# Kernel tuning notes

Hardware: AMD Instinct MI355X
Metric: run time of the kernel (lower is better)

Reference implementation:

```python
import jax, jax.numpy as jnp
import numpy as np

B, E, N, NREL, K, T, L = 8, 2000, 10000, 25, 16, 3, 32
TAU1 = 10.0

def _clip01(x):
    return jnp.clip(x, 0.0, 1.0)

def setup_inputs():
    key = jax.random.key(0)
    ks = jax.random.split(key, 10)
    ent = jax.random.randint(ks[0], (B,), 0, E)
    input_x = jnp.zeros((B, E), jnp.float32).at[jnp.arange(B), ent].set(1.0)
    tidx = jax.random.randint(ks[1], (E,), 0, K)
    type_mat = jnp.zeros((E, K), jnp.float32).at[jnp.arange(E), tidx].set(1.0)
    heads = jax.random.randint(ks[2], (N,), 0, E)
    tails = jax.random.randint(ks[3], (N,), 0, E)
    rels = jax.random.randint(ks[4], (N,), 0, NREL)
    e2triple = jnp.zeros((E, N), jnp.float32).at[heads, jnp.arange(N)].set(1.0)
    triple2e = jnp.zeros((N, E), jnp.float32).at[jnp.arange(N), tails].set(1.0)
    triple2r = jnp.zeros((N, NREL), jnp.float32).at[jnp.arange(N), rels].set(1.0)
    def ku(k, shape):
        fan_in = int(np.prod(shape[1:]))
        bnd = 1.0 / np.sqrt(fan_in)
        return jax.random.uniform(k, shape, jnp.float32, -bnd, bnd)
    w = ku(ks[5], (T, L, NREL))
    weight = ku(ks[6], (L, 1))
    h = jnp.ones((T, L, NREL - 1), jnp.float32)
    h_x = jnp.ones((L, NREL - 1), jnp.float32)
    h_type = ku(ks[7], (T, L, K))
    h_x_type = ku(ks[8], (L, K))
    alpha = jnp.ones((T, L), jnp.float32)
    beta = jnp.ones((T, L), jnp.float32)
    alpha_x = jnp.ones((L,), jnp.float32)
    beta_x = jnp.ones((L,), jnp.float32)
    return dict(input_x=input_x, type_mat=type_mat, e2triple=e2triple,
                triple2e=triple2e, triple2r=triple2r, w=w, weight=weight,
                h=h, h_x=h_x, h_type=h_type, h_x_type=h_x_type,
                alpha=alpha, beta=beta, alpha_x=alpha_x, beta_x=beta_x, flag=0)

def _forward(input_x, type_mat, e2triple, triple2e, triple2r, w, weight,
             h, h_x, h_type, h_x_type, alpha, beta, alpha_x, beta_x):
    # flag=False, is_training=False path of TCLMModel.forward
    Bb = input_x.shape[0]
    Nn, Ee = triple2e.shape
    Tt, Ll = alpha.shape
    nrel = w.shape[-1]
    half = (nrel - 1) // 2
    x_ori = input_x @ e2triple                      # [B,N]
    e2r = triple2e.T @ triple2r                     # [E,nrel]
    hidden_base = _clip01(e2r)[:, :-1]              # [E,nrel-1]
    hx_raw = _clip01(x_ori @ triple2r)              # [B,nrel]
    hidden_x_base = jnp.concatenate([hx_raw[:, half:-1], hx_raw[:, :half]], axis=-1)
    ax = _clip01(alpha_x / TAU1)
    bx = _clip01(beta_x / TAU1)
    gate_x = 1.0 - _clip01(ax + bx)                 # [L]
    hxp = _clip01(h_x / TAU1)                       # [L,nrel-1]
    hxtp = _clip01(h_x_type / TAU1)                 # [L,K]
    hidden_type_x = input_x @ (type_mat @ hxtp.T)   # [B,L]
    hx_lin = hidden_x_base @ hxp.T                  # [B,L]
    s = None
    for t in range(Tt):
        a = _clip01(alpha[t] / TAU1)                # [L]
        b = _clip01(beta[t] / TAU1)
        hp = _clip01(h[t] / TAU1)                   # [L,nrel-1]
        htp = _clip01(h_type[t] / TAU1)             # [L,K]
        hidden = _clip01(a[None] * (type_mat @ htp.T) + b[None] * (hidden_base @ hp.T))
        hidden = (hidden + (1.0 - _clip01(a + b))[None]).T        # [L,E]
        # note: original code uses alpha/beta (not alpha_x/beta_x) here; replicate
        hidden_x = _clip01(a[None] * hidden_type_x + b[None] * hx_lin) + gate_x[None]  # [B,L]
        w_probs = jax.nn.softmax(w[t], axis=-1)     # [L,nrel]
        srel = triple2r @ w_probs.T                 # [N,L]
        if t == 0:
            sc = x_ori[:, None, :] * srel.T[None]   # [B,L,N]
            s = (sc.reshape(-1, Nn) @ triple2e).reshape(Bb, Ll, Ee)
            s = s * hidden[None] * hidden_x[:, :, None]
        else:
            xprev = (s.reshape(-1, Ee) @ e2triple).reshape(Bb, Ll, Nn)
            sc = xprev * srel.T[None]               # [B,L,N]
            s = (sc.reshape(-1, Nn) @ triple2e).reshape(Bb, Ll, Ee)
            s = s * hidden[None]
    out = jnp.einsum('ble,lk->bek', s, jnp.tanh(weight))[..., 0]  # [B,E]
    return out

def reference(input_x, type_mat, e2triple, triple2e, triple2r, w, weight,
              h, h_x, h_type, h_x_type, alpha, beta, alpha_x, beta_x, flag):
    return _forward(input_x, type_mat, e2triple, triple2e, triple2r, w, weight,
                    h, h_x, h_type, h_x_type, alpha, beta, alpha_x, beta_x)
```

## Files before the change

### kernel.cpp

```cpp
#include <hip/hip_runtime.h>

#define B 8
#define E 2000
#define NTRI 10000
#define NRELS 25
#define KT 16
#define TT 3
#define LL 32
#define TAU1 10.0f
#define XBLK 8192
#define XTHR 256
#define LCAP 256

typedef __attribute__((ext_vector_type(4))) float f32x4;

__device__ __forceinline__ float clip01(float x) { return fminf(fmaxf(x, 0.0f), 1.0f); }

__global__ void __launch_bounds__(XTHR) extract_all(
        const f32x4* __restrict__ e2t, const f32x4* __restrict__ t2e,
        const float4* __restrict__ t2r, const float4* __restrict__ ix,
        const float4* __restrict__ tm, const float* __restrict__ w,
        int* __restrict__ heads, int* __restrict__ tails, int* __restrict__ rels,
        int* __restrict__ ent, int* __restrict__ tidx,
        unsigned int* __restrict__ mask_g, int* __restrict__ cnt_g,
        float* __restrict__ wrow_g, float4* __restrict__ out4) {
    const int gtid = blockIdx.x * XTHR + threadIdx.x;
    const int gs = XBLK * XTHR;

    if (gtid < 2048) mask_g[gtid] = 0u;
    if (gtid < 64) cnt_g[gtid] = 0;
    float4 z = make_float4(0.f, 0.f, 0.f, 0.f);
    for (int i = gtid; i < B * E / 4; i += gs) out4[i] = z;

    if (gtid < TT * LL) {
        const float* wr = w + gtid * NRELS;
        float mx = wr[0];
        for (int r = 1; r < NRELS; r++) mx = fmaxf(mx, wr[r]);
        float ex[NRELS], s = 0.f;
        for (int r = 0; r < NRELS; r++) { ex[r] = expf(wr[r] - mx); s += ex[r]; }
        float inv = 1.f / s;
        for (int r = 0; r < NRELS; r++) wrow_g[gtid * NRELS + r] = ex[r] * inv;
    }

    for (int i = gtid; i < B * E / 4; i += gs) {
        float4 v = ix[i];
        if (v.x != 0.f || v.y != 0.f || v.z != 0.f || v.w != 0.f) {
            float c[4] = {v.x, v.y, v.z, v.w};
#pragma unroll
            for (int k = 0; k < 4; k++)
                if (c[k] != 0.f) { int a = i * 4 + k; int bq = a / E; ent[bq] = a - bq * E; }
        }
    }
    for (int i = gtid; i < E * KT / 4; i += gs) {
        float4 v = tm[i];
        if (v.x != 0.f || v.y != 0.f || v.z != 0.f || v.w != 0.f) {
            float c[4] = {v.x, v.y, v.z, v.w};
#pragma unroll
            for (int k = 0; k < 4; k++)
                if (c[k] != 0.f) { int a = i * 4 + k; int e = a / KT; tidx[e] = a - e * KT; }
        }
    }
    for (int i = gtid; i < NTRI * NRELS / 4; i += gs) {
        float4 v = t2r[i];
        if (v.x != 0.f || v.y != 0.f || v.z != 0.f || v.w != 0.f) {
            float c[4] = {v.x, v.y, v.z, v.w};
#pragma unroll
            for (int k = 0; k < 4; k++)
                if (c[k] != 0.f) { int a = i * 4 + k; int j = a / NRELS; rels[j] = a - j * NRELS; }
        }
    }
    for (int i = gtid; i < E * NTRI / 4; i += gs) {
        f32x4 va = __builtin_nontemporal_load(&e2t[i]);
        f32x4 vb = __builtin_nontemporal_load(&t2e[i]);
        if (va.x != 0.f || va.y != 0.f || va.z != 0.f || va.w != 0.f) {
            float c[4] = {va.x, va.y, va.z, va.w};
#pragma unroll
            for (int k = 0; k < 4; k++)
                if (c[k] != 0.f) { int a = i * 4 + k; int hd = a / NTRI; heads[a - hd * NTRI] = hd; }
        }
        if (vb.x != 0.f || vb.y != 0.f || vb.z != 0.f || vb.w != 0.f) {
            float c[4] = {vb.x, vb.y, vb.z, vb.w};
#pragma unroll
            for (int k = 0; k < 4; k++)
                if (c[k] != 0.f) { int a = i * 4 + k; int j = a / E; tails[j] = a - j * E; }
        }
    }
}

__global__ void __launch_bounds__(256) build_aux(
        const int* __restrict__ heads, const int* __restrict__ tails,
        const int* __restrict__ rels, const int* __restrict__ ent,
        unsigned int* __restrict__ mask_g, int* __restrict__ cnt_g,
        int* __restrict__ list_g) {
    int j = blockIdx.x * 256 + threadIdx.x;
    if (j >= NTRI) return;
    int r = rels[j];
    if (r < NRELS - 1) atomicOr(&mask_g[tails[j]], 1u << r);
    int hd = heads[j];
#pragma unroll
    for (int q = 0; q < B; q++) {
        if (hd == ent[q]) {
            int p = atomicAdd(&cnt_g[q], 1);
            if (p < LCAP) list_g[q * LCAP + p] = j;
        }
    }
}

__global__ void __launch_bounds__(512) mega_prop(
        const int* __restrict__ heads, const int* __restrict__ tails,
        const int* __restrict__ rels, const int* __restrict__ ent,
        const int* __restrict__ tidx,
        const unsigned int* __restrict__ mask_g, const int* __restrict__ cnt_g,
        const int* __restrict__ list_g, const float* __restrict__ wrow_g,
        const float* __restrict__ h, const float* __restrict__ h_type,
        const float* __restrict__ alpha, const float* __restrict__ beta,
        const float* __restrict__ h_x, const float* __restrict__ h_x_type,
        const float* __restrict__ alpha_x, const float* __restrict__ beta_x,
        const float* __restrict__ weight, float* __restrict__ out) {
    __shared__ float prev_s[E];
    __shared__ float acc_s[E];
    __shared__ unsigned int mask_s[E];
    __shared__ int tidx_s[E];
    __shared__ float wrow_s[NRELS];
    __shared__ float hp_s[NRELS - 1];
    __shared__ float htp_s[KT];
    __shared__ float extra_sh;

    const int NT = 512;
    const int bI = blockIdx.x >> 5, l = blockIdx.x & 31, tid = threadIdx.x;
    const int ent_b = ent[bI];
    const int cnt = min(cnt_g[bI], LCAP);

    for (int e = tid; e < E; e += NT) {
        acc_s[e] = 0.f;
        mask_s[e] = mask_g[e];
        tidx_s[e] = tidx[e];
    }

    const uint4* h4 = (const uint4*)heads;
    const uint4* t4 = (const uint4*)tails;
    const uint4* r4 = (const uint4*)rels;

    for (int t = 0; t < TT; t++) {
        const int tl = t * LL + l;
        if (tid < NRELS) wrow_s[tid] = wrow_g[tl * NRELS + tid];
        if (tid >= 64 && tid < 64 + NRELS - 1)
            hp_s[tid - 64] = clip01(h[tl * (NRELS - 1) + (tid - 64)] / TAU1);
        if (tid >= 128 && tid < 128 + KT)
            htp_s[tid - 128] = clip01(h_type[tl * KT + (tid - 128)] / TAU1);
        __syncthreads();

        if (t == 0) {
            for (int i = tid; i < cnt; i += NT) {
                int j = list_g[bI * LCAP + i];
                atomicAdd(&acc_s[tails[j]], wrow_s[rels[j]]);
            }
        } else {
            for (int i = tid; i < NTRI / 4; i += NT) {
                uint4 hh = h4[i];
                float p0 = prev_s[hh.x], p1 = prev_s[hh.y];
                float p2 = prev_s[hh.z], p3 = prev_s[hh.w];
                if (p0 != 0.f || p1 != 0.f || p2 != 0.f || p3 != 0.f) {
                    uint4 tv = t4[i], rr = r4[i];
                    if (p0 != 0.f) atomicAdd(&acc_s[tv.x], p0 * wrow_s[rr.x]);
                    if (p1 != 0.f) atomicAdd(&acc_s[tv.y], p1 * wrow_s[rr.y]);
                    if (p2 != 0.f) atomicAdd(&acc_s[tv.z], p2 * wrow_s[rr.z]);
                    if (p3 != 0.f) atomicAdd(&acc_s[tv.w], p3 * wrow_s[rr.w]);
                }
            }
        }
        __syncthreads();

        const float a = clip01(alpha[tl] / TAU1);
        const float bb = clip01(beta[tl] / TAU1);
        const float base = 1.f - clip01(a + bb);

        if (t == 0 && tid == 0) {
            unsigned int fl = 0u;
            for (int i = 0; i < cnt; i++) fl |= 1u << rels[list_g[bI * LCAP + i]];
            float hxlin = 0.f;
            for (int i = 0; i < NRELS - 1; i++) {
                int pi = (i < 12) ? (12 + i) : (i - 12);
                if ((fl >> pi) & 1u) hxlin += clip01(h_x[l * (NRELS - 1) + i] / TAU1);
            }
            float htx = clip01(h_x_type[l * KT + tidx_s[ent_b]] / TAU1);
            float ax = clip01(alpha_x[l] / TAU1), bx = clip01(beta_x[l] / TAU1);
            extra_sh = clip01(a * htx + bb * hxlin) + (1.f - clip01(ax + bx));
        }
        __syncthreads();

        const float extra = (t == 0) ? extra_sh : 1.f;

        if (t < TT - 1) {
            for (int e = tid; e < E; e += NT) {
                unsigned int m = mask_s[e];
                float dot = 0.f;
#pragma unroll
                for (int i = 0; i < NRELS - 1; i++) dot += ((m >> i) & 1u) ? hp_s[i] : 0.f;
                float he = clip01(a * htp_s[tidx_s[e]] + bb * dot) + base;
                prev_s[e] = acc_s[e] * he * extra;
                acc_s[e] = 0.f;
            }
        } else {
            float tw = tanhf(weight[l]);
            for (int e = tid; e < E; e += NT) {
                unsigned int m = mask_s[e];
                float dot = 0.f;
#pragma unroll
                for (int i = 0; i < NRELS - 1; i++) dot += ((m >> i) & 1u) ? hp_s[i] : 0.f;
                float he = clip01(a * htp_s[tidx_s[e]] + bb * dot) + base;
                atomicAdd(&out[bI * E + e], acc_s[e] * he * tw);
            }
        }
        __syncthreads();
    }
}

extern "C" void kernel_launch(void* const* d_in, const int* in_sizes, int n_in,
                              void* d_out, int out_size, void* d_ws, size_t ws_size,
                              hipStream_t stream) {
    const float4* ix       = (const float4*)d_in[0];
    const float4* tm       = (const float4*)d_in[1];
    const f32x4*  e2t      = (const f32x4*)d_in[2];
    const f32x4*  t2e      = (const f32x4*)d_in[3];
    const float4* t2r      = (const float4*)d_in[4];
    const float*  w        = (const float*)d_in[5];
    const float*  weight   = (const float*)d_in[6];
    const float*  h        = (const float*)d_in[7];
    const float*  h_x      = (const float*)d_in[8];
    const float*  h_type   = (const float*)d_in[9];
    const float*  h_x_type = (const float*)d_in[10];
    const float*  alpha    = (const float*)d_in[11];
    const float*  beta     = (const float*)d_in[12];
    const float*  alpha_x  = (const float*)d_in[13];
    const float*  beta_x   = (const float*)d_in[14];
    (void)in_sizes; (void)n_in; (void)out_size; (void)ws_size;

    char* ws = (char*)d_ws;
    int* heads = (int*)ws;
    int* tails = heads + 10048;
    int* rels  = tails + 10048;
    int* ent   = rels + 10048;
    int* tidx  = ent + 64;
    unsigned int* mask_g = (unsigned int*)(tidx + 2048);
    int* cnt_g = (int*)(mask_g + 2048);
    int* list_g = cnt_g + 64;
    float* wrow_g = (float*)(list_g + B * LCAP);

    extract_all<<<XBLK, XTHR, 0, stream>>>(e2t, t2e, t2r, ix, tm, w,
                                           heads, tails, rels, ent, tidx,
                                           mask_g, cnt_g, wrow_g, (float4*)d_out);

    build_aux<<<(NTRI + 255) / 256, 256, 0, stream>>>(heads, tails, rels, ent,
                                                      mask_g, cnt_g, list_g);

    mega_prop<<<B * LL, 512, 0, stream>>>(heads, tails, rels, ent, tidx,
                                          mask_g, cnt_g, list_g, wrow_g,
                                          h, h_type, alpha, beta, h_x, h_x_type,
                                          alpha_x, beta_x, weight, (float*)d_out);
}
```

Measured before the change: 212.3 us.

## Precompute per-batch reachable-triple frontier lists for sparse propagation

Adds a per-batch build kernel that performs BFS-style reachability over the triple graph for three hops. It writes packed (head, tail, rel) lists of only the triples that can carry nonzero mass, plus the relation flags for the start entity. The propagation kernel then walks these compact lists instead of scanning all triples at hops 2 and 3, and skips zero-valued atomic adds to the output. The trade-off is a serial build kernel with only 8 blocks and a larger workspace. The packing assumes tail ids fit in 11 bits and that head ids shifted left by 16 stay within int range.

```diff
diff --git a/kernel.cpp b/kernel.cpp
--- a/kernel.cpp
+++ b/kernel.cpp
@@ -10,7 +10,6 @@
 #define TAU1 10.0f
 #define XBLK 8192
 #define XTHR 256
-#define LCAP 256
 
 typedef __attribute__((ext_vector_type(4))) float f32x4;
 
@@ -22,13 +21,10 @@
         const float4* __restrict__ tm, const float* __restrict__ w,
         int* __restrict__ heads, int* __restrict__ tails, int* __restrict__ rels,
         int* __restrict__ ent, int* __restrict__ tidx,
-        unsigned int* __restrict__ mask_g, int* __restrict__ cnt_g,
         float* __restrict__ wrow_g, float4* __restrict__ out4) {
     const int gtid = blockIdx.x * XTHR + threadIdx.x;
     const int gs = XBLK * XTHR;
 
-    if (gtid < 2048) mask_g[gtid] = 0u;
-    if (gtid < 64) cnt_g[gtid] = 0;
     float4 z = make_float4(0.f, 0.f, 0.f, 0.f);
     for (int i = gtid; i < B * E / 4; i += gs) out4[i] = z;
 
@@ -87,31 +83,75 @@
     }
 }
 
-__global__ void __launch_bounds__(256) build_aux(
+__global__ void __launch_bounds__(1024) build_all(
         const int* __restrict__ heads, const int* __restrict__ tails,
         const int* __restrict__ rels, const int* __restrict__ ent,
         unsigned int* __restrict__ mask_g, int* __restrict__ cnt_g,
-        int* __restrict__ list_g) {
-    int j = blockIdx.x * 256 + threadIdx.x;
-    if (j >= NTRI) return;
-    int r = rels[j];
-    if (r < NRELS - 1) atomicOr(&mask_g[tails[j]], 1u << r);
-    int hd = heads[j];
-#pragma unroll
-    for (int q = 0; q < B; q++) {
-        if (hd == ent[q]) {
-            int p = atomicAdd(&cnt_g[q], 1);
-            if (p < LCAP) list_g[q * LCAP + p] = j;
-        }
-    }
+        unsigned int* __restrict__ relflag_g, int* __restrict__ list_g) {
+    __shared__ unsigned int mask_s[E];
+    __shared__ unsigned int reachA[64], reachB[64];
+    __shared__ int cnt_s[TT];
+    __shared__ unsigned int rf;
+    const int b = blockIdx.x, tid = threadIdx.x;
+    const int eb = ent[b];
+
+    if (tid < 64) { reachA[tid] = 0u; reachB[tid] = 0u; }
+    if (tid < TT) cnt_s[tid] = 0;
+    if (tid == 0) rf = 0u;
+
+    if (b == 0) {
+        for (int e = tid; e < E; e += 1024) mask_s[e] = 0u;
+        __syncthreads();
+        for (int j = tid; j < NTRI; j += 1024) {
+            int r = rels[j];
+            if (r < NRELS - 1) atomicOr(&mask_s[tails[j]], 1u << r);
+        }
+        __syncthreads();
+        for (int e = tid; e < E; e += 1024) mask_g[e] = mask_s[e];
+    }
+    __syncthreads();
+
+    int* l1 = list_g + (0 * B + b) * NTRI;
+    int* l2 = list_g + (1 * B + b) * NTRI;
+    int* l3 = list_g + (2 * B + b) * NTRI;
+
+    for (int j = tid; j < NTRI; j += 1024) {
+        if (heads[j] == eb) {
+            int ta = tails[j], r = rels[j];
+            int p = atomicAdd(&cnt_s[0], 1);
+            l1[p] = (eb << 16) | (ta << 5) | r;
+            atomicOr(&reachA[ta >> 5], 1u << (ta & 31));
+            atomicOr(&rf, 1u << r);
+        }
+    }
+    __syncthreads();
+    for (int j = tid; j < NTRI; j += 1024) {
+        int hd = heads[j];
+        if ((reachA[hd >> 5] >> (hd & 31)) & 1u) {
+            int ta = tails[j];
+            int p = atomicAdd(&cnt_s[1], 1);
+            l2[p] = (hd << 16) | (ta << 5) | rels[j];
+            atomicOr(&reachB[ta >> 5], 1u << (ta & 31));
+        }
+    }
+    __syncthreads();
+    for (int j = tid; j < NTRI; j += 1024) {
+        int hd = heads[j];
+        if ((reachB[hd >> 5] >> (hd & 31)) & 1u) {
+            int p = atomicAdd(&cnt_s[2], 1);
+            l3[p] = (hd << 16) | (tails[j] << 5) | rels[j];
+        }
+    }
+    __syncthreads();
+    if (tid < TT) cnt_g[b * 4 + tid] = cnt_s[tid];
+    if (tid == 0) relflag_g[b] = rf;
 }
 
 __global__ void __launch_bounds__(512) mega_prop(
-        const int* __restrict__ heads, const int* __restrict__ tails,
-        const int* __restrict__ rels, const int* __restrict__ ent,
-        const int* __restrict__ tidx,
+        const int* __restrict__ ent, const int* __restrict__ tidx,
         const unsigned int* __restrict__ mask_g, const int* __restrict__ cnt_g,
-        const int* __restrict__ list_g, const float* __restrict__ wrow_g,
+        const unsigned int* __restrict__ relflag_g, const int* __restrict__ list_g,
+        const float* __restrict__ wrow_g,
         const float* __restrict__ h, const float* __restrict__ h_type,
         const float* __restrict__ alpha, const float* __restrict__ beta,
         const float* __restrict__ h_x, const float* __restrict__ h_x_type,
@@ -129,17 +169,12 @@
     const int NT = 512;
     const int bI = blockIdx.x >> 5, l = blockIdx.x & 31, tid = threadIdx.x;
     const int ent_b = ent[bI];
-    const int cnt = min(cnt_g[bI], LCAP);
 
     for (int e = tid; e < E; e += NT) {
         acc_s[e] = 0.f;
         mask_s[e] = mask_g[e];
         tidx_s[e] = tidx[e];
     }
-
-    const uint4* h4 = (const uint4*)heads;
-    const uint4* t4 = (const uint4*)tails;
-    const uint4* r4 = (const uint4*)rels;
 
     for (int t = 0; t < TT; t++) {
         const int tl = t * LL + l;
@@ -150,23 +185,19 @@
             htp_s[tid - 128] = clip01(h_type[tl * KT + (tid - 128)] / TAU1);
         __syncthreads();
 
+        const int cnt = cnt_g[bI * 4 + t];
+        const int* lst = list_g + (t * B + bI) * NTRI;
         if (t == 0) {
             for (int i = tid; i < cnt; i += NT) {
-                int j = list_g[bI * LCAP + i];
-                atomicAdd(&acc_s[tails[j]], wrow_s[rels[j]]);
+                int pk = lst[i];
+                atomicAdd(&acc_s[(pk >> 5) & 2047], wrow_s[pk & 31]);
             }
         } else {
-            for (int i = tid; i < NTRI / 4; i += NT) {
-                uint4 hh = h4[i];
-                float p0 = prev_s[hh.x], p1 = prev_s[hh.y];
-                float p2 = prev_s[hh.z], p3 = prev_s[hh.w];
-                if (p0 != 0.f || p1 != 0.f || p2 != 0.f || p3 != 0.f) {
-                    uint4 tv = t4[i], rr = r4[i];
-                    if (p0 != 0.f) atomicAdd(&acc_s[tv.x], p0 * wrow_s[rr.x]);
-                    if (p1 != 0.f) atomicAdd(&acc_s[tv.y], p1 * wrow_s[rr.y]);
-                    if (p2 != 0.f) atomicAdd(&acc_s[tv.z], p2 * wrow_s[rr.z]);
-                    if (p3 != 0.f) atomicAdd(&acc_s[tv.w], p3 * wrow_s[rr.w]);
-                }
+            for (int i = tid; i < cnt; i += NT) {
+                int pk = lst[i];
+                float pv = prev_s[pk >> 16];
+                if (pv != 0.f)
+                    atomicAdd(&acc_s[(pk >> 5) & 2047], pv * wrow_s[pk & 31]);
             }
         }
         __syncthreads();
@@ -176,8 +207,7 @@
         const float base = 1.f - clip01(a + bb);
 
         if (t == 0 && tid == 0) {
-            unsigned int fl = 0u;
-            for (int i = 0; i < cnt; i++) fl |= 1u << rels[list_g[bI * LCAP + i]];
+            unsigned int fl = relflag_g[bI];
             float hxlin = 0.f;
             for (int i = 0; i < NRELS - 1; i++) {
                 int pi = (i < 12) ? (12 + i) : (i - 12);
@@ -209,7 +239,8 @@
 #pragma unroll
                 for (int i = 0; i < NRELS - 1; i++) dot += ((m >> i) & 1u) ? hp_s[i] : 0.f;
                 float he = clip01(a * htp_s[tidx_s[e]] + bb * dot) + base;
-                atomicAdd(&out[bI * E + e], acc_s[e] * he * tw);
+                float v = acc_s[e] * he * tw;
+                if (v != 0.f) atomicAdd(&out[bI * E + e], v);
             }
         }
         __syncthreads();
@@ -244,18 +275,19 @@
     int* tidx  = ent + 64;
     unsigned int* mask_g = (unsigned int*)(tidx + 2048);
     int* cnt_g = (int*)(mask_g + 2048);
-    int* list_g = cnt_g + 64;
-    float* wrow_g = (float*)(list_g + B * LCAP);
+    unsigned int* relflag_g = (unsigned int*)(cnt_g + 64);
+    int* list_g = (int*)(relflag_g + 64);
+    float* wrow_g = (float*)(list_g + TT * B * NTRI);
 
     extract_all<<<XBLK, XTHR, 0, stream>>>(e2t, t2e, t2r, ix, tm, w,
                                            heads, tails, rels, ent, tidx,
-                                           mask_g, cnt_g, wrow_g, (float4*)d_out);
-
-    build_aux<<<(NTRI + 255) / 256, 256, 0, stream>>>(heads, tails, rels, ent,
-                                                      mask_g, cnt_g, list_g);
-
-    mega_prop<<<B * LL, 512, 0, stream>>>(heads, tails, rels, ent, tidx,
-                                          mask_g, cnt_g, list_g, wrow_g,
-                                          h, h_type, alpha, beta, h_x, h_x_type,
-                                          alpha_x, beta_x, weight, (float*)d_out);
-}
+                                           wrow_g, (float4*)d_out);
+
+    build_all<<<B, 1024, 0, stream>>>(heads, tails, rels, ent,
+                                      mask_g, cnt_g, relflag_g, list_g);
+
+    mega_prop<<<B * LL, 512, 0, stream>>>(ent, tidx, mask_g, cnt_g, relflag_g,
+                                          list_g, wrow_g, h, h_type, alpha, beta,
+                                          h_x, h_x_type, alpha_x, beta_x,
+                                          weight, (float*)d_out);
+}
```

After: 218.7 us. 1.03x slower.
